# Kernel tuning notes

Measured on AMD Instinct MI355X. Metric: run time of the kernel, lower is better.

The kernel has to match this reference:

```python
import jax, jax.numpy as jnp
import numpy as np

EPS = 1e-8


def _conv1(x, w):
    # x: [C,H,W], w: [O,C,k,k] -> [O,H,W] (SAME padding, stride 1)
    return jax.lax.conv_general_dilated(
        x[None], w, window_strides=(1, 1), padding='SAME',
        dimension_numbers=('NCHW', 'OIHW', 'NCHW'))[0]


def setup_inputs() -> dict:
    key = jax.random.key(0)
    k1, k2, k3, k4 = jax.random.split(key, 4)
    B, C, O, K, S, H, W = 8, 512, 512, 3, 512, 64, 64
    inp = jax.random.normal(k1, (B, C, H, W), dtype=jnp.float32)
    style = jax.random.normal(k2, (B, S), dtype=jnp.float32)
    weight = jax.random.normal(k3, (1, O, C, K, K), dtype=jnp.float32)  # conv weight
    mod_weight = jax.random.normal(k4, (C, S), dtype=jnp.float32)      # EqualLinear weight
    mod_bias = jnp.ones((C,), dtype=jnp.float32)                        # bias filled with 1.0
    return {"input": inp, "style": style, "weight": weight,
            "mod_weight": mod_weight, "mod_bias": mod_bias}


def reference(input, style, weight, mod_weight, mod_bias) -> jnp.ndarray:
    B, C, H, W = input.shape
    _, O, _, K, _ = weight.shape
    fan_in = C * K * K
    scale = 1.0 / np.sqrt(fan_in)
    lin_scale = 1.0 / np.sqrt(mod_weight.shape[1])

    # EqualLinear modulation: [B, C]
    s = style @ (mod_weight * lin_scale).T + mod_bias

    # Modulate + demodulate per-sample weights: [B, O, C, K, K]
    w = scale * weight * s[:, None, :, None, None]
    demod = jax.lax.rsqrt(jnp.sum(w * w, axis=(2, 3, 4)) + EPS)  # [B, O]
    w = w * demod[:, :, None, None, None]

    # Grouped conv with groups=B == per-sample conv, vmapped over batch
    out = jax.vmap(_conv1)(input, w)  # [B, O, H, W]
    return out
```

## Files before the change

### kernel.cpp

```cpp
#include <hip/hip_runtime.h>

typedef unsigned short u16;
typedef __bf16 bf16_t;
typedef bf16_t bf16x8 __attribute__((ext_vector_type(8)));
typedef float floatx4 __attribute__((ext_vector_type(4)));

static constexpr float kScale = 0.014731391274719741f;
static constexpr float kScale2 = 2.1701388888888894e-4f;
static constexpr float kLinScale = 0.044194173824159216f;

__device__ __forceinline__ u16 f2bf(float f) {
  unsigned u = __float_as_uint(f);
  u += 0x7FFFu + ((u >> 16) & 1u);
  return (u16)(u >> 16);
}

#define GLD16(g, l)                                                        \
  __builtin_amdgcn_global_load_lds(                                        \
      (const __attribute__((address_space(1))) unsigned int*)(g),          \
      (__attribute__((address_space(3))) unsigned int*)(l), 16, 0, 0)

__global__ __launch_bounds__(256) void k_prep1(const float* __restrict__ style,
                                               const float* __restrict__ modw,
                                               const float* __restrict__ modb,
                                               const float* __restrict__ weight,
                                               float* __restrict__ s_buf,
                                               float* __restrict__ ssq) {
  int tid = threadIdx.x;
  if (blockIdx.x < 1024) {
    int lane = tid & 63, wv = tid >> 6;
    int idx = blockIdx.x * 4 + wv;
    int b = idx >> 9, c = idx & 511;
    const float* st = style + b * 512;
    const float* mw = modw + (size_t)c * 512;
    float s = 0.f;
#pragma unroll
    for (int i = 0; i < 8; ++i) s += st[lane + i * 64] * mw[lane + i * 64];
#pragma unroll
    for (int off = 32; off; off >>= 1) s += __shfl_xor(s, off);
    if (lane == 0) s_buf[idx] = s * kLinScale + modb[c];
  } else {
    int e = (blockIdx.x - 1024) * 256 + tid;
    const float* wp = weight + (size_t)e * 9;
    float ss = 0.f;
#pragma unroll
    for (int t = 0; t < 9; ++t) ss += wp[t] * wp[t];
    ssq[e] = ss;
  }
}

__global__ __launch_bounds__(256) void k_demod2(const float* __restrict__ ssq,
                                                const float* __restrict__ s_buf,
                                                float* __restrict__ demod_buf) {
  int tid = threadIdx.x, lane = tid & 63, wv = tid >> 6;
  int idx = blockIdx.x * 4 + wv;
  int b = idx >> 9, o = idx & 511;
  const float* sq = ssq + (size_t)o * 512;
  const float* srow = s_buf + b * 512;
  float ss = 0.f;
#pragma unroll
  for (int i = 0; i < 8; ++i) {
    float s = srow[lane + i * 64];
    ss += sq[lane + i * 64] * s * s;
  }
#pragma unroll
  for (int off = 32; off; off >>= 1) ss += __shfl_xor(ss, off);
  if (lane == 0) demod_buf[idx] = rsqrtf(ss * kScale2 + 1e-8f);
}

__global__ __launch_bounds__(256) void k_transpose(const float* __restrict__ in,
                                                   const float* __restrict__ s_buf,
                                                   unsigned* __restrict__ in_t32) {
  __shared__ u16 tile[64 * 65];
  int tid = threadIdx.x;
  int c0 = blockIdx.x * 64, y = blockIdx.y, b = blockIdx.z;
  const float* src = in + ((size_t)(b * 512 + c0) * 4096) + y * 64;
  const float* srow = s_buf + b * 512 + c0;
#pragma unroll
  for (int it = 0; it < 16; ++it) {
    int idx = it * 256 + tid;
    int cl = idx >> 6, x = idx & 63;
    tile[cl * 65 + x] = f2bf(src[(size_t)cl * 4096 + x] * srow[cl]);
  }
  __syncthreads();
  unsigned* dst = in_t32 + ((size_t)(b * 64 + y) * 64) * 256 + (c0 >> 1);
#pragma unroll
  for (int it = 0; it < 8; ++it) {
    int flat = it * 256 + tid;
    int cl2 = flat & 31, x = flat >> 5;
    unsigned lo = tile[(2 * cl2) * 65 + x];
    unsigned hi = tile[(2 * cl2 + 1) * 65 + x];
    dst[(size_t)x * 256 + cl2] = lo | (hi << 16);
  }
}

__global__ __launch_bounds__(256) void k_wfrag(const float* __restrict__ weight,
                                               unsigned* __restrict__ wt32) {
  __shared__ u16 tiles[9][512];
  int tid = threadIdx.x;
  int ct = blockIdx.x, ot = blockIdx.y;
  int o0 = ot * 16, c0 = ct * 32;
#pragma unroll
  for (int i = 0; i < 18; ++i) {
    int flat = i * 256 + tid;
    int t9 = flat / 9;
    int tap = flat - t9 * 9;
    int o_l = t9 >> 5, c_l = t9 & 31;
    float w = weight[((size_t)(o0 + o_l) * 512 + c0 + c_l) * 9 + tap];
    int pos = ((o_l + ((c_l >> 3) << 4)) << 3) + (c_l & 7);
    tiles[tap][pos] = f2bf(w * kScale);
  }
  __syncthreads();
  const unsigned* tl = (const unsigned*)tiles;
#pragma unroll
  for (int tap = 0; tap < 9; ++tap)
    wt32[(size_t)((tap * 16 + ct) * 32 + ot) * 256 + tid] = tl[tap * 256 + tid];
}

__global__ __launch_bounds__(256, 3) void k_conv(const u16* __restrict__ in_t,
                                                 const u16* __restrict__ w_t,
                                                 const float* __restrict__ demod_buf,
                                                 float* __restrict__ out) {
  __shared__ char smem[33792];
  const int tid = threadIdx.x;
  const int lane = tid & 63;
  const int wv = tid >> 6;
  const int wm = wv >> 1, wn = wv & 1;
  const int quad = lane >> 4, m16 = lane & 15;
  const int lin = blockIdx.x + 32 * blockIdx.y + 128 * blockIdx.z;
  const int b = lin & 7;
  const int r_ = lin >> 3;
  const int nt = r_ & 31;
  const int mt = r_ >> 5;
  const int y0 = nt * 2;

  floatx4 acc[4][4];
#pragma unroll
  for (int i = 0; i < 4; ++i)
#pragma unroll
    for (int j = 0; j < 4; ++j) acc[i][j] = (floatx4){0.f, 0.f, 0.f, 0.f};

  const u16* abase = w_t + mt * 4096 + wm * 2048 + lane * 8;

  const int xs = tid >> 2, qs = tid & 3;
  const int qd = qs ^ ((xs >> 1) & 3);
  const u16* gB[4];
  bool rok[4];
#pragma unroll
  for (int r = 0; r < 4; ++r) {
    int y = y0 - 1 + r;
    rok[r] = (unsigned)y < 64u;
    gB[r] = in_t + (((size_t)(b * 64 + (rok[r] ? y : 0)) * 64 + xs) * 512 + qd * 8);
  }

  char* bA[3];
#pragma unroll
  for (int dx = 0; dx < 3; ++dx) {
    const int sx0 = m16 + dx - 1;
    bA[dx] = smem + wn * 4224 + (sx0 + 1) * 64 + ((quad ^ ((sx0 >> 1) & 3)) << 4);
  }

  bf16x8 aR[2][4];
  bf16x8 bv[2][4];

#define LOAD_BV(si, bufimm, t_)                                              \
  {                                                                          \
    const int dy_ = (t_) / 3, dx_ = (t_) % 3;                                \
    _Pragma("unroll") for (int ns = 0; ns < 4; ++ns)                         \
      bv[si][ns] = *(const bf16x8*)(bA[dx_] + (bufimm) + dy_ * 4224 +        \
                                    ns * 1024);                              \
  }

#define STAGE_B(bufimm)                                                      \
  {                                                                          \
    _Pragma("unroll") for (int r = 0; r < 4; ++r)                            \
      if (rok[r]) GLD16(gB[r], smem + (bufimm) + r * 4224 + 64 + wv * 1024); \
  }

#define CT_BODY(ctv, par, CURIMM, NXTIMM)                                    \
  {                                                                          \
    LOAD_BV(par, CURIMM, 0);                                                 \
    if ((ctv) + 1 < 16) {                                                    \
      _Pragma("unroll") for (int r = 0; r < 4; ++r) gB[r] += 32;             \
      STAGE_B(NXTIMM);                                                       \
    }                                                                        \
    _Pragma("unroll") for (int t = 0; t < 9; ++t) {                          \
      const int icur = (t + (par)) & 1;                                      \
      const int inxt = icur ^ 1;                                             \
      const int tp = t < 8 ? t + 1 : 0;                                      \
      const int ctp = t < 8 ? (ctv) : (ctv) + 1;                             \
      const u16* ap = abase + ((size_t)(tp * 16 + ctp) << 14);               \
      _Pragma("unroll") for (int ms = 0; ms < 4; ++ms)                       \
        aR[inxt][ms] = *(const bf16x8*)(ap + ms * 512);                      \
      if (t < 8) { LOAD_BV(inxt, CURIMM, t + 1); }                           \
      __builtin_amdgcn_s_setprio(1);                                         \
      _Pragma("unroll") for (int ns = 0; ns < 4; ++ns)                       \
        _Pragma("unroll") for (int ms = 0; ms < 4; ++ms)                     \
          acc[ms][ns] = __builtin_amdgcn_mfma_f32_16x16x32_bf16(             \
              aR[icur][ms], bv[icur][ns], acc[ms][ns], 0, 0, 0);             \
      __builtin_amdgcn_s_setprio(0);                                         \
    }                                                                        \
    asm volatile("s_waitcnt vmcnt(4)" ::: "memory");                         \
    __builtin_amdgcn_s_barrier();                                            \
  }

  {
    const uint4 z = make_uint4(0u, 0u, 0u, 0u);
    for (int i = tid; i < 2112; i += 256) ((uint4*)smem)[i] = z;
  }
  __syncthreads();
  STAGE_B(0);
  __syncthreads();
#pragma unroll
  for (int ms = 0; ms < 4; ++ms)
    aR[0][ms] = *(const bf16x8*)(abase + ms * 512);

  for (int ct = 0; ct < 16; ct += 2) {
    CT_BODY(ct, 0, 0, 16896);
    CT_BODY(ct + 1, 1, 16896, 0);
  }

#undef LOAD_BV
#undef STAGE_B
#undef CT_BODY

  const int ob = mt * 128 + wm * 64;
  const int nb = nt * 128 + wn * 64;
#pragma unroll
  for (int ms = 0; ms < 4; ++ms)
#pragma unroll
    for (int ns = 0; ns < 4; ++ns) {
      const int n = nb + ns * 16 + m16;
#pragma unroll
      for (int r = 0; r < 4; ++r) {
        const int o = ob + ms * 16 + quad * 4 + r;
        float dm = demod_buf[b * 512 + o];
        out[((size_t)(b * 512 + o) << 12) + n] = acc[ms][ns][r] * dm;
      }
    }
}

extern "C" void kernel_launch(void* const* d_in, const int* in_sizes, int n_in,
                              void* d_out, int out_size, void* d_ws, size_t ws_size,
                              hipStream_t stream) {
  const float* input = (const float*)d_in[0];
  const float* style = (const float*)d_in[1];
  const float* weight = (const float*)d_in[2];
  const float* modw = (const float*)d_in[3];
  const float* modb = (const float*)d_in[4];
  float* out = (float*)d_out;
  char* ws = (char*)d_ws;
  float* s_buf = (float*)ws;
  float* demod_buf = (float*)(ws + 16384);
  float* ssq = (float*)(ws + 32768);
  u16* in_t = (u16*)(ws + 32768 + 1048576);
  u16* w_t = (u16*)(ws + 32768 + 1048576 + 33554432);

  k_prep1<<<dim3(2048), dim3(256), 0, stream>>>(style, modw, modb, weight, s_buf, ssq);
  k_demod2<<<dim3(1024), dim3(256), 0, stream>>>(ssq, s_buf, demod_buf);
  k_transpose<<<dim3(8, 64, 8), dim3(256), 0, stream>>>(input, s_buf, (unsigned*)in_t);
  k_wfrag<<<dim3(16, 32), dim3(256), 0, stream>>>(weight, (unsigned*)w_t);
  k_conv<<<dim3(32, 4, 8), dim3(256), 0, stream>>>(in_t, w_t, demod_buf, out);
}
```

Measured before the change: 253.6 us.

## Double the channel chunk per pipeline stage to 64 in conv kernel

```diff
diff --git a/kernel.cpp b/kernel.cpp
--- a/kernel.cpp
+++ b/kernel.cpp
@@ -117,11 +117,11 @@
     wt32[(size_t)((tap * 16 + ct) * 32 + ot) * 256 + tid] = tl[tap * 256 + tid];
 }
 
-__global__ __launch_bounds__(256, 3) void k_conv(const u16* __restrict__ in_t,
+__global__ __launch_bounds__(256, 2) void k_conv(const u16* __restrict__ in_t,
                                                  const u16* __restrict__ w_t,
                                                  const float* __restrict__ demod_buf,
                                                  float* __restrict__ out) {
-  __shared__ char smem[33792];
+  __shared__ char smem[67584];
   const int tid = threadIdx.x;
   const int lane = tid & 63;
   const int wv = tid >> 6;
@@ -142,46 +142,64 @@
 
   const u16* abase = w_t + mt * 4096 + wm * 2048 + lane * 8;
 
-  const int xs = tid >> 2, qs = tid & 3;
-  const int qd = qs ^ ((xs >> 1) & 3);
+  const int xs = tid >> 3, qs = tid & 7;
+  const int cch = qs ^ (xs & 7);
   const u16* gB[4];
   bool rok[4];
 #pragma unroll
   for (int r = 0; r < 4; ++r) {
     int y = y0 - 1 + r;
     rok[r] = (unsigned)y < 64u;
-    gB[r] = in_t + (((size_t)(b * 64 + (rok[r] ? y : 0)) * 64 + xs) * 512 + qd * 8);
-  }
-
-  char* bA[3];
+    gB[r] = in_t + (((size_t)(b * 64 + (rok[r] ? y : 0)) * 64 + xs) * 512 + cch * 8);
+  }
+
+  char* bA[6];
 #pragma unroll
   for (int dx = 0; dx < 3; ++dx) {
     const int sx0 = m16 + dx - 1;
-    bA[dx] = smem + wn * 4224 + (sx0 + 1) * 64 + ((quad ^ ((sx0 >> 1) & 3)) << 4);
-  }
-
-  bf16x8 aR[2][4];
-  bf16x8 bv[2][4];
+#pragma unroll
+    for (int kh = 0; kh < 2; ++kh)
+      bA[dx * 2 + kh] = smem + wn * 8448 + (sx0 + 1) * 128 +
+                        (((kh * 4 + quad) ^ (sx0 & 7)) << 4);
+  }
+
+  bf16x8 aR[2][2][4];
+  bf16x8 bv[2][2][4];
 
 #define LOAD_BV(si, bufimm, t_)                                              \
   {                                                                          \
     const int dy_ = (t_) / 3, dx_ = (t_) % 3;                                \
-    _Pragma("unroll") for (int ns = 0; ns < 4; ++ns)                         \
-      bv[si][ns] = *(const bf16x8*)(bA[dx_] + (bufimm) + dy_ * 4224 +        \
-                                    ns * 1024);                              \
+    _Pragma("unroll") for (int kh = 0; kh < 2; ++kh)                         \
+      _Pragma("unroll") for (int ns = 0; ns < 4; ++ns)                       \
+        bv[si][kh][ns] = *(const bf16x8*)(bA[dx_ * 2 + kh] + (bufimm) +      \
+                                          dy_ * 8448 + ns * 2048);           \
   }
 
 #define STAGE_B(bufimm)                                                      \
   {                                                                          \
     _Pragma("unroll") for (int r = 0; r < 4; ++r)                            \
-      if (rok[r]) GLD16(gB[r], smem + (bufimm) + r * 4224 + 64 + wv * 1024); \
+      if (rok[r]) {                                                          \
+        GLD16(gB[r], smem + (bufimm) + r * 8448 + 128 + wv * 1024);          \
+        GLD16(gB[r] + 16384,                                                 \
+              smem + (bufimm) + r * 8448 + 128 + 4096 + wv * 1024);          \
+      }                                                                      \
+  }
+
+#define LOAD_A2(si, tp_, ctp_)                                               \
+  {                                                                          \
+    _Pragma("unroll") for (int kh = 0; kh < 2; ++kh) {                       \
+      const u16* ap_ =                                                       \
+          abase + ((size_t)((tp_)*16 + 2 * (ctp_) + kh) << 14);              \
+      _Pragma("unroll") for (int ms = 0; ms < 4; ++ms)                       \
+        aR[si][kh][ms] = *(const bf16x8*)(ap_ + ms * 512);                   \
+    }                                                                        \
   }
 
 #define CT_BODY(ctv, par, CURIMM, NXTIMM)                                    \
   {                                                                          \
     LOAD_BV(par, CURIMM, 0);                                                 \
-    if ((ctv) + 1 < 16) {                                                    \
-      _Pragma("unroll") for (int r = 0; r < 4; ++r) gB[r] += 32;             \
+    if ((ctv) + 1 < 8) {                                                     \
+      _Pragma("unroll") for (int r = 0; r < 4; ++r) gB[r] += 64;             \
       STAGE_B(NXTIMM);                                                       \
     }                                                                        \
     _Pragma("unroll") for (int t = 0; t < 9; ++t) {                          \
@@ -189,39 +207,37 @@
       const int inxt = icur ^ 1;                                             \
       const int tp = t < 8 ? t + 1 : 0;                                      \
       const int ctp = t < 8 ? (ctv) : (ctv) + 1;                             \
-      const u16* ap = abase + ((size_t)(tp * 16 + ctp) << 14);               \
-      _Pragma("unroll") for (int ms = 0; ms < 4; ++ms)                       \
-        aR[inxt][ms] = *(const bf16x8*)(ap + ms * 512);                      \
+      LOAD_A2(inxt, tp, ctp);                                                \
       if (t < 8) { LOAD_BV(inxt, CURIMM, t + 1); }                           \
       __builtin_amdgcn_s_setprio(1);                                         \
-      _Pragma("unroll") for (int ns = 0; ns < 4; ++ns)                       \
-        _Pragma("unroll") for (int ms = 0; ms < 4; ++ms)                     \
-          acc[ms][ns] = __builtin_amdgcn_mfma_f32_16x16x32_bf16(             \
-              aR[icur][ms], bv[icur][ns], acc[ms][ns], 0, 0, 0);             \
+      _Pragma("unroll") for (int kh = 0; kh < 2; ++kh)                       \
+        _Pragma("unroll") for (int ns = 0; ns < 4; ++ns)                     \
+          _Pragma("unroll") for (int ms = 0; ms < 4; ++ms)                   \
+            acc[ms][ns] = __builtin_amdgcn_mfma_f32_16x16x32_bf16(           \
+                aR[icur][kh][ms], bv[icur][kh][ns], acc[ms][ns], 0, 0, 0);   \
       __builtin_amdgcn_s_setprio(0);                                         \
     }                                                                        \
-    asm volatile("s_waitcnt vmcnt(4)" ::: "memory");                         \
+    asm volatile("s_waitcnt vmcnt(8)" ::: "memory");                         \
     __builtin_amdgcn_s_barrier();                                            \
   }
 
   {
     const uint4 z = make_uint4(0u, 0u, 0u, 0u);
-    for (int i = tid; i < 2112; i += 256) ((uint4*)smem)[i] = z;
+    for (int i = tid; i < 4224; i += 256) ((uint4*)smem)[i] = z;
   }
   __syncthreads();
   STAGE_B(0);
   __syncthreads();
-#pragma unroll
-  for (int ms = 0; ms < 4; ++ms)
-    aR[0][ms] = *(const bf16x8*)(abase + ms * 512);
-
-  for (int ct = 0; ct < 16; ct += 2) {
-    CT_BODY(ct, 0, 0, 16896);
-    CT_BODY(ct + 1, 1, 16896, 0);
+  LOAD_A2(0, 0, 0);
+
+  for (int ct = 0; ct < 8; ct += 2) {
+    CT_BODY(ct, 0, 0, 33792);
+    CT_BODY(ct + 1, 1, 33792, 0);
   }
 
 #undef LOAD_BV
 #undef STAGE_B
+#undef LOAD_A2
 #undef CT_BODY
 
   const int ob = mt * 128 + wm * 64;
```

Measured after the change: 249.3 us. No clear change (-1.7%).

## Drop register double-buffering of MFMA operands and raise occupancy to 4 waves/SIMD

Applied to the files above, without the earlier changes.

```diff
diff --git a/kernel.cpp b/kernel.cpp
--- a/kernel.cpp
+++ b/kernel.cpp
@@ -117,7 +117,7 @@
     wt32[(size_t)((tap * 16 + ct) * 32 + ot) * 256 + tid] = tl[tap * 256 + tid];
 }
 
-__global__ __launch_bounds__(256, 3) void k_conv(const u16* __restrict__ in_t,
+__global__ __launch_bounds__(256, 4) void k_conv(const u16* __restrict__ in_t,
                                                  const u16* __restrict__ w_t,
                                                  const float* __restrict__ demod_buf,
                                                  float* __restrict__ out) {
@@ -160,48 +160,37 @@
     bA[dx] = smem + wn * 4224 + (sx0 + 1) * 64 + ((quad ^ ((sx0 >> 1) & 3)) << 4);
   }
 
-  bf16x8 aR[2][4];
-  bf16x8 bv[2][4];
-
-#define LOAD_BV(si, bufimm, t_)                                              \
-  {                                                                          \
-    const int dy_ = (t_) / 3, dx_ = (t_) % 3;                                \
-    _Pragma("unroll") for (int ns = 0; ns < 4; ++ns)                         \
-      bv[si][ns] = *(const bf16x8*)(bA[dx_] + (bufimm) + dy_ * 4224 +        \
-                                    ns * 1024);                              \
-  }
-
 #define STAGE_B(bufimm)                                                      \
   {                                                                          \
     _Pragma("unroll") for (int r = 0; r < 4; ++r)                            \
       if (rok[r]) GLD16(gB[r], smem + (bufimm) + r * 4224 + 64 + wv * 1024); \
   }
 
-#define CT_BODY(ctv, par, CURIMM, NXTIMM)                                    \
+#define CT_BODY(ctv, CURIMM, NXTIMM)                                         \
   {                                                                          \
-    LOAD_BV(par, CURIMM, 0);                                                 \
     if ((ctv) + 1 < 16) {                                                    \
       _Pragma("unroll") for (int r = 0; r < 4; ++r) gB[r] += 32;             \
       STAGE_B(NXTIMM);                                                       \
     }                                                                        \
     _Pragma("unroll") for (int t = 0; t < 9; ++t) {                          \
-      const int icur = (t + (par)) & 1;                                      \
-      const int inxt = icur ^ 1;                                             \
-      const int tp = t < 8 ? t + 1 : 0;                                      \
-      const int ctp = t < 8 ? (ctv) : (ctv) + 1;                             \
-      const u16* ap = abase + ((size_t)(tp * 16 + ctp) << 14);               \
-      _Pragma("unroll") for (int ms = 0; ms < 4; ++ms)                       \
-        aR[inxt][ms] = *(const bf16x8*)(ap + ms * 512);                      \
-      if (t < 8) { LOAD_BV(inxt, CURIMM, t + 1); }                           \
+      const int dy_ = t / 3, dx_ = t % 3;                                    \
+      bf16x8 aF[4], bF[4];                                                   \
+      {                                                                      \
+        const u16* ap_ = abase + ((size_t)(t * 16 + (ctv)) << 14);           \
+        _Pragma("unroll") for (int ms = 0; ms < 4; ++ms)                     \
+          aF[ms] = *(const bf16x8*)(ap_ + ms * 512);                         \
+      }                                                                      \
+      _Pragma("unroll") for (int ns = 0; ns < 4; ++ns)                       \
+        bF[ns] = *(const bf16x8*)(bA[dx_] + (CURIMM) + dy_ * 4224 +          \
+                                  ns * 1024);                                \
       __builtin_amdgcn_s_setprio(1);                                         \
       _Pragma("unroll") for (int ns = 0; ns < 4; ++ns)                       \
         _Pragma("unroll") for (int ms = 0; ms < 4; ++ms)                     \
           acc[ms][ns] = __builtin_amdgcn_mfma_f32_16x16x32_bf16(             \
-              aR[icur][ms], bv[icur][ns], acc[ms][ns], 0, 0, 0);             \
+              aF[ms], bF[ns], acc[ms][ns], 0, 0, 0);                         \
       __builtin_amdgcn_s_setprio(0);                                         \
     }                                                                        \
-    asm volatile("s_waitcnt vmcnt(4)" ::: "memory");                         \
-    __builtin_amdgcn_s_barrier();                                            \
+    __syncthreads();       \
   }
 
   {
@@ -211,16 +200,12 @@
   __syncthreads();
   STAGE_B(0);
   __syncthreads();
-#pragma unroll
-  for (int ms = 0; ms < 4; ++ms)
-    aR[0][ms] = *(const bf16x8*)(abase + ms * 512);
 
   for (int ct = 0; ct < 16; ct += 2) {
-    CT_BODY(ct, 0, 0, 16896);
-    CT_BODY(ct + 1, 1, 16896, 0);
-  }
-
-#undef LOAD_BV
+    CT_BODY(ct, 0, 16896);
+    CT_BODY(ct + 1, 16896, 0);
+  }
+
 #undef STAGE_B
 #undef CT_BODY
 
```

Measured after the change: 270.7 us. 6.8% more time.
